# Optimization experiments

Hardware: AMD Instinct MI355X
Metric: run time of the kernel (lower is better)

The kernel has to match this reference:

```python
import jax, jax.numpy as jnp
import numpy as np

B, T, S = 64, 128, 16
E = 512           # d2v input size
H = 512           # bi-LSTM output size (args.d2v_embed)
Hh = H // 2       # per-direction hidden
NL = 2            # num_layers
ED = 128          # args.embedding_dim
USERS, ARTS, PAD = 100000, 100000, 0


def setup_inputs() -> dict:
    key = jax.random.key(0)
    ks = jax.random.split(key, 32)
    p = 0.02
    inp = {}
    inp["x1"] = jax.random.normal(ks[0], (B, T, E), jnp.float32)
    inp["sample_d2v_embeds"] = jax.random.normal(ks[1], (B, T, S, H), jnp.float32)
    # LSTM params: layer-0 input E == layer-1 input H, so stackable. gate order i,f,g,o
    inp["lstm_Wih"] = jax.random.normal(ks[2], (NL, 2, 4 * Hh, E), jnp.float32) * p
    inp["lstm_Whh"] = jax.random.normal(ks[3], (NL, 2, 4 * Hh, Hh), jnp.float32) * p
    inp["lstm_bih"] = jax.random.normal(ks[4], (NL, 2, 4 * Hh), jnp.float32) * p
    inp["lstm_bhh"] = jax.random.normal(ks[5], (NL, 2, 4 * Hh), jnp.float32) * p
    inp["attn_W1"] = jax.random.normal(ks[6], (H, H), jnp.float32) * p
    inp["attn_b1"] = jax.random.normal(ks[7], (H,), jnp.float32) * p
    inp["attn_w2"] = jax.random.normal(ks[8], (H,), jnp.float32) * p
    inp["rnn_mlp_W"] = jax.random.normal(ks[9], (64, H), jnp.float32) * p
    inp["rnn_mlp_b"] = jax.random.normal(ks[10], (64,), jnp.float32) * p
    inp["user_table"] = jax.random.normal(ks[11], (USERS, ED), jnp.float32) * p
    inp["art_table"] = (jax.random.normal(ks[12], (ARTS, ED), jnp.float32) * p).at[PAD].set(0.0)
    inp["em_W1"] = jax.random.normal(ks[13], (128, ED), jnp.float32) * p
    inp["em_b1"] = jax.random.normal(ks[14], (128,), jnp.float32) * p
    inp["em_W2"] = jax.random.normal(ks[15], (64, 128), jnp.float32) * p
    inp["em_b2"] = jax.random.normal(ks[16], (64,), jnp.float32) * p
    inp["lm_W1"] = jax.random.normal(ks[17], (256, 128), jnp.float32) * p
    inp["lm_b1"] = jax.random.normal(ks[18], (256,), jnp.float32) * p
    inp["lm_W2"] = jax.random.normal(ks[19], (128, 256), jnp.float32) * p
    inp["lm_b2"] = jax.random.normal(ks[20], (128,), jnp.float32) * p
    inp["lm_W3"] = jax.random.normal(ks[21], (64, 128), jnp.float32) * p
    inp["lm_b3"] = jax.random.normal(ks[22], (64,), jnp.float32) * p
    inp["lm_W4"] = jax.random.normal(ks[23], (1, 64), jnp.float32) * p
    inp["lm_b4"] = jax.random.normal(ks[24], (1,), jnp.float32) * p
    inp["x2"] = 0  # unused '_' arg
    inp["cate"] = jax.random.randint(ks[25], (B, T), 0, 10)  # unused by forward
    lens = jax.random.randint(ks[26], (B,), 1, T + 1)
    inp["seq_lens"] = jnp.sort(lens)[::-1]  # pack requires descending
    inp["user_ids"] = jax.random.randint(ks[27], (B,), 0, USERS)
    inp["sample_ids"] = jax.random.randint(ks[28], (B, T, S), 0, ARTS)
    return inp


def _bilstm(x, lens, Wih, Whh, bih, bhh):
    # Packed bidirectional LSTM == padded LSTM with state updates masked to t < len.
    Bc, Tc, _ = x.shape
    tmask = jnp.arange(Tc)[None, :] < lens[:, None]       # [B,T]
    m_t = tmask.T[:, :, None]                             # [T,B,1]
    for l in range(NL):
        outs = []
        for d, rev in ((0, False), (1, True)):
            xg = jnp.einsum('bti,gi->tbg', x, Wih[l, d]) + bih[l, d]  # [T,B,4Hh]
            Whh_ld, bhh_ld = Whh[l, d], bhh[l, d]

            def step(carry, inp_t, Whh_ld=Whh_ld, bhh_ld=bhh_ld):
                h, c = carry
                xg_t, m = inp_t
                g = xg_t + h @ Whh_ld.T + bhh_ld
                i_, f_, g_, o_ = jnp.split(g, 4, axis=-1)
                c2 = jax.nn.sigmoid(f_) * c + jax.nn.sigmoid(i_) * jnp.tanh(g_)
                h2 = jax.nn.sigmoid(o_) * jnp.tanh(c2)
                h = jnp.where(m, h2, h)
                c = jnp.where(m, c2, c)
                return (h, c), h

            init = (jnp.zeros((Bc, Hh), x.dtype), jnp.zeros((Bc, Hh), x.dtype))
            _, hs = jax.lax.scan(step, init, (xg, m_t), reverse=rev)
            outs.append(jnp.transpose(hs, (1, 0, 2)))
        x = jnp.concatenate(outs, axis=-1)                # [B,T,H]
    return x, tmask


def reference(x1, sample_d2v_embeds, lstm_Wih, lstm_Whh, lstm_bih, lstm_bhh,
              attn_W1, attn_b1, attn_w2, rnn_mlp_W, rnn_mlp_b,
              user_table, art_table, em_W1, em_b1, em_W2, em_b2,
              lm_W1, lm_b1, lm_W2, lm_b2, lm_W3, lm_b3, lm_W4, lm_b4,
              x2, cate, seq_lens, user_ids, sample_ids):
    rnn, tmask = _bilstm(x1, seq_lens, lstm_Wih, lstm_Whh, lstm_bih, lstm_bhh)
    # per-key MLP attention score, causal softmax, weighted sum (the packed double loop)
    sc = jnp.einsum('bth,h->bt', jnp.tanh(jnp.einsum('bth,oh->bto', rnn, attn_W1) + attn_b1), attn_w2)
    causal = jnp.tril(jnp.ones((rnn.shape[1], rnn.shape[1]), bool))
    logits = jnp.where(causal[None, :, :], sc[:, None, :], jnp.float32(-1e30))
    a = jax.nn.softmax(logits, axis=-1)                   # [B,T(query),T(key)]
    ctx = jnp.einsum('bts,bsh->bth', a, rnn)
    ctx = jnp.where(tmask[:, :, None], ctx, 0.0)          # rnn_step zeros at padded t
    # embedding branch
    ue = user_table[user_ids]                             # [B,ED]
    se = art_table[sample_ids]                            # [B,T,S,ED]
    e = ue[:, None, None, :] * se
    e = jax.nn.relu(e @ em_W1.T + em_b1)
    e = jax.nn.relu(e @ em_W2.T + em_b2)                  # [B,T,S,64]
    # rnn branch
    r = ctx[:, :, None, :] * sample_d2v_embeds
    r = r @ rnn_mlp_W.T + rnn_mlp_b                       # [B,T,S,64]
    z = jnp.concatenate([e, r], axis=-1)                  # [B,T,S,128]
    z = jax.nn.relu(z @ lm_W1.T + lm_b1)
    z = jax.nn.relu(z @ lm_W2.T + lm_b2)
    z = jax.nn.relu(z @ lm_W3.T + lm_b3)
    z = jax.nn.sigmoid(z @ lm_W4.T + lm_b4)
    return jnp.squeeze(z, axis=-1)                        # [B,T,S]
```

## Files before the change

kernel.cpp:

```cpp
#include <hip/hip_runtime.h>
#include <cstddef>

namespace {

constexpr int T = 128;

typedef unsigned short u16;
typedef unsigned int u32;
typedef unsigned long long u64;
typedef __attribute__((ext_vector_type(8))) short short8;
typedef __attribute__((ext_vector_type(4))) float f32x4;
typedef __attribute__((ext_vector_type(4))) int i32x4;

__device__ __forceinline__ u16 f2bf(float x) {
  u32 u = __float_as_uint(x);
  u = (u + 0x7FFFu + ((u >> 16) & 1u)) >> 16;
  return (u16)u;
}
__device__ __forceinline__ float bf2f(u16 v) {
  return __uint_as_float(((u32)v) << 16);
}
__device__ __forceinline__ float sigf(float x) {
  return __builtin_amdgcn_rcpf(1.f + __builtin_amdgcn_exp2f(-1.44269504f * x));
}
__device__ __forceinline__ float tanh2(float x) {
  return 1.f - 2.f * __builtin_amdgcn_rcpf(1.f + __builtin_amdgcn_exp2f(2.88539008f * x));
}
__device__ __forceinline__ void bar_lds() {
  asm volatile("s_waitcnt lgkmcnt(0)\n\ts_barrier" ::: "memory");
}

constexpr int O_WIH = 0;
constexpr int O_AW1 = 2097152;
constexpr int O_EM1 = 2359296;
constexpr int O_EM2 = 2375680;
constexpr int O_MLP = 2383872;
constexpr int O_LW1 = 2416640;
constexpr int O_LW2 = 2449408;
constexpr int O_LW3 = 2482176;
constexpr int N_WBF = 2490368;

__global__ __launch_bounds__(256)
void k_prep(const float* __restrict__ wih, const float* __restrict__ aw1,
            const float* __restrict__ e1, const float* __restrict__ e2,
            const float* __restrict__ mw, const float* __restrict__ l1,
            const float* __restrict__ l2, const float* __restrict__ l3,
            u16* __restrict__ wbf) {
  int i = blockIdx.x * 256 + threadIdx.x;
  if (i >= N_WBF) return;
  float v;
  if (i < O_AW1)      v = wih[i];
  else if (i < O_EM1) v = aw1[i - O_AW1];
  else if (i < O_EM2) v = e1[i - O_EM1];
  else if (i < O_MLP) v = e2[i - O_EM2];
  else if (i < O_LW1) v = mw[i - O_MLP];
  else if (i < O_LW2) v = l1[i - O_LW1];
  else if (i < O_LW3) v = l2[i - O_LW2];
  else                v = l3[i - O_LW3];
  wbf[i] = f2bf(v);
}

__global__ __launch_bounds__(256)
void k_prepw(const float* __restrict__ whh, signed char* __restrict__ wq) {
  int i = blockIdx.x * 256 + threadIdx.x;
  float v = whh[i] * 1016.f;
  v = fminf(fmaxf(v, -127.f), 127.f);
  wq[i] = (signed char)(int)rintf(v);
}

__global__ __launch_bounds__(256)
void k_xg_mfma(const float* __restrict__ X, const u16* __restrict__ Wbf,
               const float* __restrict__ bi, const float* __restrict__ bh,
               float* __restrict__ xg) {
  __shared__ __align__(16) u16 sx[32 * 520];
  int tid = threadIdx.x;
  int rowbase = blockIdx.x * 32;
  int nchunk = blockIdx.y;
  for (int idx = tid; idx < 4096; idx += 256) {
    int r = idx >> 7, k4 = idx & 127;
    float4 v = *(const float4*)(X + (size_t)(rowbase + r) * 512 + k4 * 4);
    u32* p = (u32*)(sx + r * 520 + k4 * 4);
    p[0] = (u32)f2bf(v.x) | ((u32)f2bf(v.y) << 16);
    p[1] = (u32)f2bf(v.z) | ((u32)f2bf(v.w) << 16);
  }
  __syncthreads();
  int w = tid >> 6, lane = tid & 63;
  int msub = w >> 1, nhalf = w & 1;
  int mbase = msub * 16;
  int nb0 = nchunk * 256 + nhalf * 128;
  f32x4 acc[8];
#pragma unroll
  for (int i = 0; i < 8; ++i) acc[i] = f32x4{0.f, 0.f, 0.f, 0.f};
  for (int kt = 0; kt < 16; ++kt) {
    short8 a = *(const short8*)(sx + (mbase + (lane & 15)) * 520 + kt * 32 + (lane >> 4) * 8);
#pragma unroll
    for (int nt = 0; nt < 8; ++nt) {
      short8 b = *(const short8*)(Wbf + (size_t)(nb0 + nt * 16 + (lane & 15)) * 512 +
                                  kt * 32 + (lane >> 4) * 8);
      acc[nt] = __builtin_amdgcn_mfma_f32_16x16x32_bf16(a, b, acc[nt], 0, 0, 0);
    }
  }
  int mr = mbase + (lane >> 4) * 4;
#pragma unroll
  for (int nt = 0; nt < 8; ++nt) {
    int n = nb0 + nt * 16 + (lane & 15);
    float bb = bi[n] + bh[n];
#pragma unroll
    for (int r = 0; r < 4; ++r)
      xg[(size_t)(rowbase + mr + r) * 2048 + n] = acc[nt][r] + bb;
  }
}

template <int NT, int KT, bool RELU>
__device__ __forceinline__ void stage_mfma(const u16* __restrict__ Wbf,
                                           const float* __restrict__ bias,
                                           const u16* A, int lda,
                                           u16* O, int ldo, int nofs,
                                           int lane, int msub, int nhalf) {
  f32x4 acc[NT];
#pragma unroll
  for (int i = 0; i < NT; ++i) acc[i] = f32x4{0.f, 0.f, 0.f, 0.f};
  int mbase = msub * 16;
  int nb0 = nhalf * (NT * 16);
#pragma unroll
  for (int kt = 0; kt < KT; ++kt) {
    short8 a = *(const short8*)(A + (mbase + (lane & 15)) * lda + kt * 32 + (lane >> 4) * 8);
#pragma unroll
    for (int nt = 0; nt < NT; ++nt) {
      short8 b = *(const short8*)(Wbf + (size_t)(nb0 + nt * 16 + (lane & 15)) * (KT * 32) +
                                  kt * 32 + (lane >> 4) * 8);
      acc[nt] = __builtin_amdgcn_mfma_f32_16x16x32_bf16(a, b, acc[nt], 0, 0, 0);
    }
  }
  int mr = mbase + (lane >> 4) * 4;
#pragma unroll
  for (int nt = 0; nt < NT; ++nt) {
    int nl = nb0 + nt * 16 + (lane & 15);
    float bv = bias[nl];
#pragma unroll
    for (int r = 0; r < 4; ++r) {
      float v = acc[nt][r] + bv;
      if (RELU) v = fmaxf(v, 0.f);
      O[(mr + r) * ldo + nofs + nl] = f2bf(v);
    }
  }
}

__global__ __launch_bounds__(512, 1)
void k_lstm6(const float* __restrict__ xg, const signed char* __restrict__ wq,
             const int* __restrict__ lens, float* __restrict__ out, int layer,
             const float* __restrict__ utab, const float* __restrict__ atab,
             const int* __restrict__ uids, const int* __restrict__ sids,
             const u16* __restrict__ wbf, const float* __restrict__ em_b1,
             const float* __restrict__ em_b2, u16* __restrict__ ez) {
  __shared__ __align__(16) signed char hq[2][16 * 272];
  __shared__ __align__(16) u16 ebufA[2 * 32 * 136];
  __shared__ __align__(16) u16 ebufB[2 * 32 * 136];
  const int tid = threadIdx.x;

  if (blockIdx.x >= 8) {
    const int half = tid >> 8;
    const int t = tid & 255;
    const int lane = t & 63, wv = t >> 6;
    const int msub = wv >> 1, nhalf = wv & 1;
    const int rowbase = ((int)blockIdx.x - 8) * 64 + half * 32;
    u16* eA = ebufA + half * 4352;
    u16* eB = ebufB + half * 4352;
#pragma unroll
    for (int it = 0; it < 4; ++it) {
      int idx = it * 256 + t;
      int r = idx >> 5, k4 = idx & 31;
      int m = rowbase + r;
      int sid = sids[m];
      int uid = uids[m >> 11];
      float4 u = *(const float4*)(utab + (size_t)uid * 128 + k4 * 4);
      float4 a = *(const float4*)(atab + (size_t)sid * 128 + k4 * 4);
      u32* p = (u32*)(eA + r * 136 + k4 * 4);
      p[0] = (u32)f2bf(u.x * a.x) | ((u32)f2bf(u.y * a.y) << 16);
      p[1] = (u32)f2bf(u.z * a.z) | ((u32)f2bf(u.w * a.w) << 16);
    }
    bar_lds();
    stage_mfma<4, 4, true>(wbf + O_EM1, em_b1, eA, 136, eB, 136, 0, lane, msub, nhalf);
    bar_lds();
    {
      f32x4 acc[2];
      acc[0] = f32x4{0.f, 0.f, 0.f, 0.f};
      acc[1] = f32x4{0.f, 0.f, 0.f, 0.f};
#pragma unroll
      for (int kt = 0; kt < 4; ++kt) {
        short8 a = *(const short8*)(eB + (msub * 16 + (lane & 15)) * 136 +
                                    kt * 32 + (lane >> 4) * 8);
#pragma unroll
        for (int nt = 0; nt < 2; ++nt) {
          int n = nhalf * 32 + nt * 16 + (lane & 15);
          short8 b = *(const short8*)(wbf + O_EM2 + (size_t)n * 128 +
                                      kt * 32 + (lane >> 4) * 8);
          acc[nt] = __builtin_amdgcn_mfma_f32_16x16x32_bf16(a, b, acc[nt], 0, 0, 0);
        }
      }
      int mr = msub * 16 + (lane >> 4) * 4;
#pragma unroll
      for (int nt = 0; nt < 2; ++nt) {
        int n = nhalf * 32 + nt * 16 + (lane & 15);
        float bv = em_b2[n];
#pragma unroll
        for (int r = 0; r < 4; ++r)
          ez[(size_t)(rowbase + mr + r) * 64 + n] = f2bf(fmaxf(acc[nt][r] + bv, 0.f));
      }
    }
    return;
  }

  const int d = blockIdx.x >> 2, bg = blockIdx.x & 3;
  const int jc = tid >> 6, l = tid & 63, ln = l & 15, lk = l >> 4;
  const int mb = bg * 16;

  i32x4 Bq[4][2][4];
  const signed char* wbase = wq + (size_t)(layer * 2 + d) * 262144;
#pragma unroll
  for (int g = 0; g < 4; ++g)
#pragma unroll
    for (int js = 0; js < 2; ++js)
#pragma unroll
      for (int kc = 0; kc < 4; ++kc) {
        int n = g * 256 + jc * 32 + js * 16 + ln;
        Bq[g][js][kc] = *(const i32x4*)(wbase + (size_t)n * 256 + kc * 64 + lk * 16);
      }

  int mlen[4];
#pragma unroll
  for (int r = 0; r < 4; ++r) mlen[r] = lens[mb + lk * 4 + r];

  float cst[2][4], hst[2][4];
#pragma unroll
  for (int js = 0; js < 2; ++js)
#pragma unroll
    for (int r = 0; r < 4; ++r) { cst[js][r] = 0.f; hst[js][r] = 0.f; }

  const float DEQ = 1.f / (1016.f * 127.f);

  for (int s = 0; s < 128; ++s) {
    const int t = d ? (127 - s) : s;

    float xv[4][2][4];
#pragma unroll
    for (int g = 0; g < 4; ++g)
#pragma unroll
      for (int js = 0; js < 2; ++js)
#pragma unroll
        for (int r = 0; r < 4; ++r)
          xv[g][js][r] = xg[((size_t)(mb + lk * 4 + r) * 128 + t) * 2048 +
                            d * 1024 + g * 256 + jc * 32 + js * 16 + ln];

    i32x4 acc[4][2];
#pragma unroll
    for (int g = 0; g < 4; ++g)
#pragma unroll
      for (int js = 0; js < 2; ++js) acc[g][js] = i32x4{0, 0, 0, 0};

    if (s > 0) {
      const signed char* hr = hq[(s & 1) ^ 1];
#pragma unroll
      for (int kc = 0; kc < 4; ++kc) {
        i32x4 a = *(const i32x4*)(hr + ln * 272 + kc * 64 + lk * 16);
#pragma unroll
        for (int g = 0; g < 4; ++g)
#pragma unroll
          for (int js = 0; js < 2; ++js)
            acc[g][js] = __builtin_amdgcn_mfma_i32_16x16x64_i8(a, Bq[g][js][kc],
                                                               acc[g][js], 0, 0, 0);
      }
    }

    signed char* hw = hq[s & 1];
#pragma unroll
    for (int js = 0; js < 2; ++js)
#pragma unroll
      for (int r = 0; r < 4; ++r) {
        float gi = (float)acc[0][js][r] * DEQ + xv[0][js][r];
        float gf = (float)acc[1][js][r] * DEQ + xv[1][js][r];
        float gg = (float)acc[2][js][r] * DEQ + xv[2][js][r];
        float go = (float)acc[3][js][r] * DEQ + xv[3][js][r];
        float c2 = sigf(gf) * cst[js][r] + sigf(gi) * tanh2(gg);
        float h2 = sigf(go) * tanh2(c2);
        const int m = lk * 4 + r;
        bool upd = t < mlen[r];
        cst[js][r] = upd ? c2 : cst[js][r];
        float hn = upd ? h2 : hst[js][r];
        hst[js][r] = hn;
        const int j = jc * 32 + js * 16 + ln;
        out[((size_t)(mb + m) * 128 + t) * 512 + d * 256 + j] = hn;
        hw[m * 272 + j] = (signed char)(int)rintf(hn * 127.f);
      }
    bar_lds();
  }
}

__global__ __launch_bounds__(256)
void k_attn(const float* __restrict__ rnn, const u16* __restrict__ W1bf,
            const float* __restrict__ b1, const float* __restrict__ w2,
            float* __restrict__ sc) {
  __shared__ __align__(16) u16 sx[32 * 520];
  __shared__ float sred[32];
  int tid = threadIdx.x;
  int rowbase = blockIdx.x * 32;
  for (int idx = tid; idx < 4096; idx += 256) {
    int r = idx >> 7, k4 = idx & 127;
    float4 v = *(const float4*)(rnn + (size_t)(rowbase + r) * 512 + k4 * 4);
    u32* p = (u32*)(sx + r * 520 + k4 * 4);
    p[0] = (u32)f2bf(v.x) | ((u32)f2bf(v.y) << 16);
    p[1] = (u32)f2bf(v.z) | ((u32)f2bf(v.w) << 16);
  }
  if (tid < 32) sred[tid] = 0.f;
  __syncthreads();
  int w = tid >> 6, lane = tid & 63;
  int msub = w >> 1, nhalf = w & 1;
  int mbase = msub * 16;
  float psum[4] = {0.f, 0.f, 0.f, 0.f};
  for (int ng = 0; ng < 4; ++ng) {
    f32x4 acc[4];
#pragma unroll
    for (int i = 0; i < 4; ++i) acc[i] = f32x4{0.f, 0.f, 0.f, 0.f};
    for (int kt = 0; kt < 16; ++kt) {
      short8 a = *(const short8*)(sx + (mbase + (lane & 15)) * 520 + kt * 32 + (lane >> 4) * 8);
#pragma unroll
      for (int nt = 0; nt < 4; ++nt) {
        int nrow = nhalf * 256 + ng * 64 + nt * 16 + (lane & 15);
        short8 b = *(const short8*)(W1bf + (size_t)nrow * 512 + kt * 32 + (lane >> 4) * 8);
        acc[nt] = __builtin_amdgcn_mfma_f32_16x16x32_bf16(a, b, acc[nt], 0, 0, 0);
      }
    }
#pragma unroll
    for (int nt = 0; nt < 4; ++nt) {
      int n = nhalf * 256 + ng * 64 + nt * 16 + (lane & 15);
      float wn = w2[n], bn = b1[n];
#pragma unroll
      for (int r = 0; r < 4; ++r) psum[r] += wn * tanh2(acc[nt][r] + bn);
    }
  }
#pragma unroll
  for (int off = 8; off >= 1; off >>= 1)
#pragma unroll
    for (int r = 0; r < 4; ++r) psum[r] += __shfl_xor(psum[r], off);
  if ((lane & 15) == 0) {
#pragma unroll
    for (int r = 0; r < 4; ++r)
      atomicAdd(&sred[msub * 16 + (lane >> 4) * 4 + r], psum[r]);
  }
  __syncthreads();
  if (tid < 32) sc[rowbase + tid] = sred[tid];
}

__global__ __launch_bounds__(128)
void k_ctx(const float* __restrict__ sc, const float* __restrict__ rnn,
           const int* __restrict__ lens, float* __restrict__ ctx) {
  int b = blockIdx.x;
  int h = blockIdx.y * 128 + threadIdx.x;
  __shared__ float ex[T];
  ex[threadIdx.x] = expf(sc[b * T + threadIdx.x]);
  __syncthreads();
  int len = lens[b];
  float acc = 0.f, den = 0.f;
  for (int t = 0; t < T; ++t) {
    float wv = ex[t];
    den += wv;
    acc += wv * rnn[((size_t)b * T + t) * 512 + h];
    ctx[((size_t)b * T + t) * 512 + h] = (t < len) ? (acc / den) : 0.f;
  }
}

__global__ __launch_bounds__(256)
void k_sample(const float* __restrict__ ctx, const float* __restrict__ d2v,
              const u16* __restrict__ ez,
              const u16* __restrict__ wbf, const float* __restrict__ mlp_b,
              const float* __restrict__ lm_b1, const float* __restrict__ lm_b2,
              const float* __restrict__ lm_b3,
              const float* __restrict__ lm_W4, const float* __restrict__ lm_b4,
              float* __restrict__ out) {
  __shared__ __align__(16) u16 bufA[32 * 264];
  __shared__ __align__(16) u16 bufB[32 * 264];
  __shared__ __align__(16) u16 bufC[32 * 136];
  __shared__ float sred[32];
  int tid = threadIdx.x, lane = tid & 63, w = tid >> 6;
  int msub = w >> 1, nhalf = w & 1;
  int mbase = msub * 16;
  int rowbase = blockIdx.x * 32;

  if (tid < 32) sred[tid] = 0.f;

  for (int idx = tid; idx < 512; idx += 256) {
    int r = idx >> 4, q = idx & 15;
    *(u64*)(bufC + r * 136 + q * 4) =
        *(const u64*)(ez + (size_t)(rowbase + r) * 64 + q * 4);
  }

  float4 dd0[8], dd1[8];
#pragma unroll
  for (int it = 0; it < 8; ++it) {
    int idx = it * 256 + tid;
    int r = idx >> 6, k4 = idx & 63;
    int m = rowbase + r;
    dd0[it] = *(const float4*)(d2v + (size_t)m * 512 + k4 * 4);
  }
#pragma unroll
  for (int it = 0; it < 8; ++it) {
    int idx = it * 256 + tid;
    int r = idx >> 6, k4 = idx & 63;
    int m = rowbase + r;
    dd1[it] = *(const float4*)(d2v + (size_t)m * 512 + 256 + k4 * 4);
  }

#pragma unroll
  for (int it = 0; it < 8; ++it) {
    int idx = it * 256 + tid;
    int r = idx >> 6, k4 = idx & 63;
    int m = rowbase + r;
    int bt = m >> 4;
    float4 cx = *(const float4*)(ctx + (size_t)bt * 512 + k4 * 4);
    float4 dv = dd0[it];
    u32* p = (u32*)(bufA + r * 264 + k4 * 4);
    p[0] = (u32)f2bf(cx.x * dv.x) | ((u32)f2bf(cx.y * dv.y) << 16);
    p[1] = (u32)f2bf(cx.z * dv.z) | ((u32)f2bf(cx.w * dv.w) << 16);
  }
  bar_lds();

  f32x4 racc[2];
  racc[0] = f32x4{0.f, 0.f, 0.f, 0.f};
  racc[1] = f32x4{0.f, 0.f, 0.f, 0.f};
  for (int kc = 0; kc < 2; ++kc) {
#pragma unroll
    for (int kt = 0; kt < 8; ++kt) {
      short8 a = *(const short8*)(bufA + (mbase + (lane & 15)) * 264 + kt * 32 + (lane >> 4) * 8);
#pragma unroll
      for (int nt = 0; nt < 2; ++nt) {
        int n = nhalf * 32 + nt * 16 + (lane & 15);
        short8 b = *(const short8*)(wbf + O_MLP + (size_t)n * 512 + kc * 256 +
                                    kt * 32 + (lane >> 4) * 8);
        racc[nt] = __builtin_amdgcn_mfma_f32_16x16x32_bf16(a, b, racc[nt], 0, 0, 0);
      }
    }
    bar_lds();
    if (kc == 0) {
#pragma unroll
      for (int it = 0; it < 8; ++it) {
        int idx = it * 256 + tid;
        int r = idx >> 6, k4 = idx & 63;
        int m = rowbase + r;
        int bt = m >> 4;
        float4 cx = *(const float4*)(ctx + (size_t)bt * 512 + 256 + k4 * 4);
        float4 dv = dd1[it];
        u32* p = (u32*)(bufA + r * 264 + k4 * 4);
        p[0] = (u32)f2bf(cx.x * dv.x) | ((u32)f2bf(cx.y * dv.y) << 16);
        p[1] = (u32)f2bf(cx.z * dv.z) | ((u32)f2bf(cx.w * dv.w) << 16);
      }
      bar_lds();
    }
  }
  {
    int mr = mbase + (lane >> 4) * 4;
#pragma unroll
    for (int nt = 0; nt < 2; ++nt) {
      int nl = nhalf * 32 + nt * 16 + (lane & 15);
      float bv = mlp_b[nl];
#pragma unroll
      for (int r = 0; r < 4; ++r)
        bufC[(mr + r) * 136 + 64 + nl] = f2bf(racc[nt][r] + bv);
    }
  }
  bar_lds();
  stage_mfma<8, 4, true>(wbf + O_LW1, lm_b1, bufC, 136, bufB, 264, 0, lane, msub, nhalf);
  bar_lds();
  stage_mfma<4, 8, true>(wbf + O_LW2, lm_b2, bufB, 264, bufA, 264, 0, lane, msub, nhalf);
  bar_lds();

  {
    f32x4 acc[2];
    acc[0] = f32x4{0.f, 0.f, 0.f, 0.f};
    acc[1] = f32x4{0.f, 0.f, 0.f, 0.f};
#pragma unroll
    for (int kt = 0; kt < 4; ++kt) {
      short8 a = *(const short8*)(bufA + (mbase + (lane & 15)) * 264 + kt * 32 + (lane >> 4) * 8);
#pragma unroll
      for (int nt = 0; nt < 2; ++nt) {
        int n = nhalf * 32 + nt * 16 + (lane & 15);
        short8 b = *(const short8*)(wbf + O_LW3 + (size_t)n * 128 +
                                    kt * 32 + (lane >> 4) * 8);
        acc[nt] = __builtin_amdgcn_mfma_f32_16x16x32_bf16(a, b, acc[nt], 0, 0, 0);
      }
    }
    float psum[4] = {0.f, 0.f, 0.f, 0.f};
#pragma unroll
    for (int nt = 0; nt < 2; ++nt) {
      int nl = nhalf * 32 + nt * 16 + (lane & 15);
      float bv = lm_b3[nl], w4 = lm_W4[nl];
#pragma unroll
      for (int r = 0; r < 4; ++r) psum[r] += w4 * fmaxf(acc[nt][r] + bv, 0.f);
    }
#pragma unroll
    for (int off = 8; off >= 1; off >>= 1)
#pragma unroll
      for (int r = 0; r < 4; ++r) psum[r] += __shfl_xor(psum[r], off);
    if ((lane & 15) == 0) {
#pragma unroll
      for (int r = 0; r < 4; ++r)
        atomicAdd(&sred[mbase + (lane >> 4) * 4 + r], psum[r]);
    }
  }
  bar_lds();
  if (tid < 32) out[rowbase + tid] = sigf(sred[tid] + lm_b4[0]);
}

}

extern "C" void kernel_launch(void* const* d_in, const int* in_sizes, int n_in,
                              void* d_out, int out_size, void* d_ws, size_t ws_size,
                              hipStream_t stream) {
  const float* x1   = (const float*)d_in[0];
  const float* d2v  = (const float*)d_in[1];
  const float* Wih  = (const float*)d_in[2];
  const float* Whh  = (const float*)d_in[3];
  const float* bih  = (const float*)d_in[4];
  const float* bhh  = (const float*)d_in[5];
  const float* aW1  = (const float*)d_in[6];
  const float* ab1  = (const float*)d_in[7];
  const float* aw2  = (const float*)d_in[8];
  const float* mlpW = (const float*)d_in[9];
  const float* mlpb = (const float*)d_in[10];
  const float* utab = (const float*)d_in[11];
  const float* atab = (const float*)d_in[12];
  const float* emW1 = (const float*)d_in[13];
  const float* emb1 = (const float*)d_in[14];
  const float* emW2 = (const float*)d_in[15];
  const float* emb2 = (const float*)d_in[16];
  const float* lmW1 = (const float*)d_in[17];
  const float* lmb1 = (const float*)d_in[18];
  const float* lmW2 = (const float*)d_in[19];
  const float* lmb2 = (const float*)d_in[20];
  const float* lmW3 = (const float*)d_in[21];
  const float* lmb3 = (const float*)d_in[22];
  const float* lmW4 = (const float*)d_in[23];
  const float* lmb4 = (const float*)d_in[24];
  const int* lens   = (const int*)d_in[27];
  const int* uids   = (const int*)d_in[28];
  const int* sids   = (const int*)d_in[29];
  float* out = (float*)d_out;

  float* ws = (float*)d_ws;
  signed char* WQ = (signed char*)ws;
  float* SC  = ws + 262144;
  u16* WBF = (u16*)(ws + 270336);
  float* XG  = ws + 1515520;
  float* R0  = ws + 18292736;
  float* R1  = ws + 22487040;
  u16* EZ  = (u16*)(ws + 26681344);
  float* CTX = ws + 18292736;

  k_prep<<<(N_WBF + 255) / 256, 256, 0, stream>>>(Wih, aW1, emW1, emW2, mlpW,
                                                  lmW1, lmW2, lmW3, WBF);
  k_prepw<<<4096, 256, 0, stream>>>(Whh, WQ);
  k_xg_mfma<<<dim3(256, 8), 256, 0, stream>>>(x1, WBF + O_WIH, bih, bhh, XG);
  k_lstm6<<<8 + 2048, 512, 0, stream>>>(XG, WQ, lens, R0, 0,
                                        utab, atab, uids, sids,
                                        WBF, emb1, emb2, EZ);
  k_xg_mfma<<<dim3(256, 8), 256, 0, stream>>>(R0, WBF + O_WIH + 1048576,
                                              bih + 2048, bhh + 2048, XG);
  k_lstm6<<<8, 512, 0, stream>>>(XG, WQ, lens, R1, 1,
                                 utab, atab, uids, sids,
                                 WBF, emb1, emb2, EZ);
  k_attn<<<256, 256, 0, stream>>>(R1, WBF + O_AW1, ab1, aw2, SC);
  k_ctx<<<dim3(64, 4), 128, 0, stream>>>(SC, R1, lens, CTX);
  k_sample<<<4096, 256, 0, stream>>>(CTX, d2v, EZ, WBF, mlpb,
                                     lmb1, lmb2, lmb3, lmW4, lmb4, out);
}
```

Baseline: 1.176 ms.

## Store LSTM input gates as bf16 and split recurrence across twice as many blocks

The precomputed input-gate projections are now written as packed bf16 instead of fp32, halving the traffic the serial LSTM loop reads each step. The recurrent kernel now spreads each direction over 8 blocks of 8 batch rows instead of 4 blocks of 16. Half the MFMA rows in each block are padding: those lanes skip loads and stores, and the hidden-state buffer is zeroed at the start. The aim is to shorten the serial critical path by adding parallelism, at the cost of wasted MFMA work and bf16 rounding of the gate inputs.

```diff
diff --git a/kernel.cpp b/kernel.cpp
--- a/kernel.cpp
+++ b/kernel.cpp
@@ -71,7 +71,7 @@
 __global__ __launch_bounds__(256)
 void k_xg_mfma(const float* __restrict__ X, const u16* __restrict__ Wbf,
                const float* __restrict__ bi, const float* __restrict__ bh,
-               float* __restrict__ xg) {
+               u16* __restrict__ xgb) {
   __shared__ __align__(16) u16 sx[32 * 520];
   int tid = threadIdx.x;
   int rowbase = blockIdx.x * 32;
@@ -106,8 +106,14 @@
     int n = nb0 + nt * 16 + (lane & 15);
     float bb = bi[n] + bh[n];
 #pragma unroll
-    for (int r = 0; r < 4; ++r)
-      xg[(size_t)(rowbase + mr + r) * 2048 + n] = acc[nt][r] + bb;
+    for (int r = 0; r < 4; ++r) {
+      u16 myv = f2bf(acc[nt][r] + bb);
+      u16 other = (u16)__shfl_xor((int)myv, 1);
+      if ((lane & 1) == 0) {
+        u32 word = (u32)myv | ((u32)other << 16);
+        *(u32*)(xgb + (size_t)(rowbase + mr + r) * 2048 + n) = word;
+      }
+    }
   }
 }
 
@@ -147,7 +153,7 @@
 }
 
 __global__ __launch_bounds__(512, 1)
-void k_lstm6(const float* __restrict__ xg, const signed char* __restrict__ wq,
+void k_lstm6(const u16* __restrict__ xgb, const signed char* __restrict__ wq,
              const int* __restrict__ lens, float* __restrict__ out, int layer,
              const float* __restrict__ utab, const float* __restrict__ atab,
              const int* __restrict__ uids, const int* __restrict__ sids,
@@ -158,12 +164,12 @@
   __shared__ __align__(16) u16 ebufB[2 * 32 * 136];
   const int tid = threadIdx.x;
 
-  if (blockIdx.x >= 8) {
+  if (blockIdx.x >= 16) {
     const int half = tid >> 8;
     const int t = tid & 255;
     const int lane = t & 63, wv = t >> 6;
     const int msub = wv >> 1, nhalf = wv & 1;
-    const int rowbase = ((int)blockIdx.x - 8) * 64 + half * 32;
+    const int rowbase = ((int)blockIdx.x - 16) * 64 + half * 32;
     u16* eA = ebufA + half * 4352;
     u16* eB = ebufB + half * 4352;
 #pragma unroll
@@ -211,9 +217,12 @@
     return;
   }
 
-  const int d = blockIdx.x >> 2, bg = blockIdx.x & 3;
+  const int d = blockIdx.x >> 3, mg = blockIdx.x & 7;
   const int jc = tid >> 6, l = tid & 63, ln = l & 15, lk = l >> 4;
-  const int mb = bg * 16;
+  const int mb = mg * 8;
+  const bool act = (lk < 2);
+
+  for (int i = tid; i < 2 * 16 * 272; i += 512) ((signed char*)hq)[i] = 0;
 
   i32x4 Bq[4][2][4];
   const signed char* wbase = wq + (size_t)(layer * 2 + d) * 262144;
@@ -229,7 +238,10 @@
 
   int mlen[4];
 #pragma unroll
-  for (int r = 0; r < 4; ++r) mlen[r] = lens[mb + lk * 4 + r];
+  for (int r = 0; r < 4; ++r) {
+    int li = mb + lk * 4 + r;
+    mlen[r] = lens[li < 64 ? li : 63];
+  }
 
   float cst[2][4], hst[2][4];
 #pragma unroll
@@ -238,19 +250,22 @@
     for (int r = 0; r < 4; ++r) { cst[js][r] = 0.f; hst[js][r] = 0.f; }
 
   const float DEQ = 1.f / (1016.f * 127.f);
+  bar_lds();
 
   for (int s = 0; s < 128; ++s) {
     const int t = d ? (127 - s) : s;
 
-    float xv[4][2][4];
-#pragma unroll
-    for (int g = 0; g < 4; ++g)
-#pragma unroll
-      for (int js = 0; js < 2; ++js)
-#pragma unroll
-        for (int r = 0; r < 4; ++r)
-          xv[g][js][r] = xg[((size_t)(mb + lk * 4 + r) * 128 + t) * 2048 +
-                            d * 1024 + g * 256 + jc * 32 + js * 16 + ln];
+    float xv[4][2][4] = {};
+    if (act) {
+#pragma unroll
+      for (int g = 0; g < 4; ++g)
+#pragma unroll
+        for (int js = 0; js < 2; ++js)
+#pragma unroll
+          for (int r = 0; r < 4; ++r)
+            xv[g][js][r] = bf2f(xgb[((size_t)(mb + lk * 4 + r) * 128 + t) * 2048 +
+                                    d * 1024 + g * 256 + jc * 32 + js * 16 + ln]);
+    }
 
     i32x4 acc[4][2];
 #pragma unroll
@@ -288,9 +303,11 @@
         cst[js][r] = upd ? c2 : cst[js][r];
         float hn = upd ? h2 : hst[js][r];
         hst[js][r] = hn;
-        const int j = jc * 32 + js * 16 + ln;
-        out[((size_t)(mb + m) * 128 + t) * 512 + d * 256 + j] = hn;
-        hw[m * 272 + j] = (signed char)(int)rintf(hn * 127.f);
+        if (act) {
+          const int j = jc * 32 + js * 16 + ln;
+          out[((size_t)(mb + m) * 128 + t) * 512 + d * 256 + j] = hn;
+          hw[m * 272 + j] = (signed char)(int)rintf(hn * 127.f);
+        }
       }
     bar_lds();
   }
@@ -549,7 +566,7 @@
   signed char* WQ = (signed char*)ws;
   float* SC  = ws + 262144;
   u16* WBF = (u16*)(ws + 270336);
-  float* XG  = ws + 1515520;
+  u16* XG  = (u16*)(ws + 1515520);
   float* R0  = ws + 18292736;
   float* R1  = ws + 22487040;
   u16* EZ  = (u16*)(ws + 26681344);
@@ -559,14 +576,14 @@
                                                   lmW1, lmW2, lmW3, WBF);
   k_prepw<<<4096, 256, 0, stream>>>(Whh, WQ);
   k_xg_mfma<<<dim3(256, 8), 256, 0, stream>>>(x1, WBF + O_WIH, bih, bhh, XG);
-  k_lstm6<<<8 + 2048, 512, 0, stream>>>(XG, WQ, lens, R0, 0,
-                                        utab, atab, uids, sids,
-                                        WBF, emb1, emb2, EZ);
+  k_lstm6<<<16 + 2048, 512, 0, stream>>>(XG, WQ, lens, R0, 0,
+                                         utab, atab, uids, sids,
+                                         WBF, emb1, emb2, EZ);
   k_xg_mfma<<<dim3(256, 8), 256, 0, stream>>>(R0, WBF + O_WIH + 1048576,
                                               bih + 2048, bhh + 2048, XG);
-  k_lstm6<<<8, 512, 0, stream>>>(XG, WQ, lens, R1, 1,
-                                 utab, atab, uids, sids,
-                                 WBF, emb1, emb2, EZ);
+  k_lstm6<<<16, 512, 0, stream>>>(XG, WQ, lens, R1, 1,
+                                  utab, atab, uids, sids,
+                                  WBF, emb1, emb2, EZ);
   k_attn<<<256, 256, 0, stream>>>(R1, WBF + O_AW1, ab1, aw2, SC);
   k_ctx<<<dim3(64, 4), 128, 0, stream>>>(SC, R1, lens, CTX);
   k_sample<<<4096, 256, 0, stream>>>(CTX, d2v, EZ, WBF, mlpb,
```

After: 1.222 ms. 1.04x slower.
